# Kernel optimization log

Measured on AMD Instinct MI355X. Metric: run time of the kernel, lower is better.

## Reference

```python
import jax, jax.numpy as jnp
import numpy as np

N_NODES = 50000


def gat_layer(x, src, dst, W, att_s, att_d, b, concat):
    # PyG GATConv (eval mode): h = x W reshaped to [N, H, C]
    H, C = att_s.shape
    h = (x @ W).reshape(-1, H, C)                      # [N, H, C]
    a_s = (h * att_s).sum(-1)                          # [N, H]
    a_d = (h * att_d).sum(-1)                          # [N, H]
    e = jax.nn.leaky_relu(a_s[src] + a_d[dst], 0.2)    # [E, H]
    # scatter-softmax over destination nodes
    m = jax.ops.segment_max(e, dst, num_segments=N_NODES)
    alpha = jnp.exp(e - m[dst])
    denom = jax.ops.segment_sum(alpha, dst, num_segments=N_NODES)
    alpha = alpha / denom[dst]                         # [E, H]
    msg = h[src] * alpha[:, :, None]                   # [E, H, C]
    out = jax.ops.segment_sum(msg, dst, num_segments=N_NODES)  # [N, H, C]
    out = out.reshape(N_NODES, H * C) if concat else out.mean(axis=1)
    return out + b


def setup_inputs() -> dict:
    key = jax.random.key(0)
    ks = jax.random.split(key, 16)
    F_IN, HID, HEADS, NCLS, E = 512, 64, 4, 40, 800000
    x = jax.random.normal(ks[0], (N_NODES, F_IN), dtype=jnp.float32)
    edge_index = jax.random.randint(ks[1], (2, E), 0, N_NODES, dtype=jnp.int32)

    def glorot(k, shape):
        fan = shape[0]
        return jax.random.normal(k, shape, dtype=jnp.float32) / np.sqrt(fan)

    d1 = HID * HEADS  # 256
    return {
        "x": x,
        "edge_index": edge_index,
        "W1": glorot(ks[2], (F_IN, d1)),
        "as1": glorot(ks[3], (HEADS, HID)),
        "ad1": glorot(ks[4], (HEADS, HID)),
        "b1": jnp.zeros((d1,), jnp.float32),
        "W2": glorot(ks[5], (d1, d1)),
        "as2": glorot(ks[6], (HEADS, HID)),
        "ad2": glorot(ks[7], (HEADS, HID)),
        "b2": jnp.zeros((d1,), jnp.float32),
        "W3": glorot(ks[8], (d1, NCLS)),
        "as3": glorot(ks[9], (1, NCLS)),
        "ad3": glorot(ks[10], (1, NCLS)),
        "b3": jnp.zeros((NCLS,), jnp.float32),
    }


def reference(x, edge_index, W1, as1, ad1, b1, W2, as2, ad2, b2, W3, as3, ad3, b3):
    # add self-loops (PyG GATConv default)
    loops = jnp.arange(N_NODES, dtype=edge_index.dtype)
    src = jnp.concatenate([edge_index[0], loops])
    dst = jnp.concatenate([edge_index[1], loops])
    h = jax.nn.elu(gat_layer(x, src, dst, W1, as1, ad1, b1, True))
    h = jax.nn.elu(gat_layer(h, src, dst, W2, as2, ad2, b2, True))
    out = gat_layer(h, src, dst, W3, as3, ad3, b3, False)
    return out
```

## Files before the change

### kernel.cpp

```cpp
#include <hip/hip_runtime.h>
#include <stdint.h>

#define NN 50000
#define NB 196

typedef unsigned short u16;
typedef _Float16 f16;
typedef __attribute__((ext_vector_type(8))) _Float16 half8;
typedef __attribute__((ext_vector_type(4))) _Float16 half4;
typedef __attribute__((ext_vector_type(4))) float f32x4;

__device__ __forceinline__ void gload_lds16(const void* gsrc, void* ldst){
  __builtin_amdgcn_global_load_lds(
      (const __attribute__((address_space(1))) unsigned int*)gsrc,
      (__attribute__((address_space(3))) unsigned int*)ldst,
      16, 0, 0);
}

#define VMW(N)  asm volatile("s_waitcnt vmcnt(" #N ")" ::: "memory")
#define LGKM0() asm volatile("s_waitcnt lgkmcnt(0)" ::: "memory")
#define BARR()  asm volatile("s_barrier" ::: "memory")


__global__ void count_k(const int* __restrict__ dst, int* __restrict__ cnt, int E){
  int i = blockIdx.x * 256 + threadIdx.x;
  int tot = E + NN;
  if (i >= tot) return;
  int d = (i < E) ? dst[i] : (i - E);
  atomicAdd(&cnt[d], 1);
}

__global__ __launch_bounds__(256) void scan_part_k(const int* __restrict__ cnt,
                                                   int* __restrict__ bsum){
  __shared__ int lds[256];
  int tid = threadIdx.x;
  int idx = blockIdx.x * 256 + tid;
  lds[tid] = (idx < NN) ? cnt[idx] : 0;
  __syncthreads();
#pragma unroll
  for (int off = 128; off >= 1; off >>= 1){
    if (tid < off) lds[tid] += lds[tid + off];
    __syncthreads();
  }
  if (tid == 0) bsum[blockIdx.x] = lds[0];
}

__global__ __launch_bounds__(256) void scan_top_k(const int* __restrict__ bsum,
                                                  int* __restrict__ boff,
                                                  int* __restrict__ row_ptr){
  __shared__ int lds[256];
  int tid = threadIdx.x;
  int v = (tid < NB) ? bsum[tid] : 0;
  lds[tid] = v;
  __syncthreads();
#pragma unroll
  for (int off = 1; off < 256; off <<= 1){
    int t = (tid >= off) ? lds[tid - off] : 0;
    __syncthreads();
    lds[tid] += t;
    __syncthreads();
  }
  if (tid < NB) boff[tid] = lds[tid] - v;
  if (tid == 255) row_ptr[NN] = lds[255];
}

__global__ __launch_bounds__(256) void scan_fin_k(const int* __restrict__ cnt,
                                                  const int* __restrict__ boff,
                                                  int* __restrict__ row_ptr,
                                                  int* __restrict__ cursor){
  __shared__ int lds[256];
  int tid = threadIdx.x;
  int idx = blockIdx.x * 256 + tid;
  int v = (idx < NN) ? cnt[idx] : 0;
  lds[tid] = v;
  __syncthreads();
#pragma unroll
  for (int off = 1; off < 256; off <<= 1){
    int t = (tid >= off) ? lds[tid - off] : 0;
    __syncthreads();
    lds[tid] += t;
    __syncthreads();
  }
  if (idx < NN){
    int r = boff[blockIdx.x] + lds[tid] - v;
    row_ptr[idx] = r;
    cursor[idx]  = r;
  }
}

__global__ void scatter_k(const int* __restrict__ src, const int* __restrict__ dst,
                          int* __restrict__ cursor, int* __restrict__ csr,
                          int* __restrict__ csrd, int E){
  int i = blockIdx.x * 256 + threadIdx.x;
  int tot = E + NN;
  if (i >= tot) return;
  int s, d;
  if (i < E){ s = src[i]; d = dst[i]; } else { s = i - E; d = i - E; }
  int pos = atomicAdd(&cursor[d], 1);
  csr[pos] = s;
  csrd[pos] = d;
}


__global__ void transpose_k(const float* __restrict__ W, f16* __restrict__ Wt, int K, int N){
  int i = blockIdx.x * 256 + threadIdx.x;
  if (i >= K * N) return;
  int n = i / K, k = i - n * K;
  Wt[i] = (f16)W[k * N + n];
}


template<bool A_FP32>
__global__ __launch_bounds__(512) void gemm_big_k(const void* __restrict__ Aptr,
                                                  const f16* __restrict__ Bt,
                                                  f16* __restrict__ C,
                                                  const float* __restrict__ atts,
                                                  const float* __restrict__ attd,
                                                  float* __restrict__ a_s,
                                                  float* __restrict__ a_d,
                                                  int M, int K){
  constexpr int ABYTES = A_FP32 ? 16384 : 8192;
  constexpr int STEPB  = ABYTES + 16384;
  __shared__ __attribute__((aligned(16))) char lds[2 * STEPB];

  const int tid  = threadIdx.x;
  const int wave = tid >> 6, lane = tid & 63;
  const int quad = lane >> 4, l16 = lane & 15;
  const int wm = wave >> 2, wn = wave & 3;
  const int m0 = blockIdx.x * 128;
  const int sc_l = lane >> 4, r_l = lane & 15;

  const size_t bsrc0 = (size_t)(wave * 16 + r_l) * K + sc_l * 8;
  const size_t bsrc1 = (size_t)((wave + 8) * 16 + r_l) * K + sc_l * 8;
  const int bdst0 = wave * 1024;
  const int bdst1 = (wave + 8) * 1024;

  int arow = m0 + wave * 16 + r_l; if (arow > M - 1) arow = M - 1;
  const size_t asrc0 = (size_t)arow * K + sc_l * 8;
  const size_t asrc1 = asrc0 + 4;
  const int adst0 = wave * 1024;
  const int adst1 = 8192 + wave * 1024;

  auto stage = [&](int buf, int k0){
    char* Ab = lds + buf * STEPB;
    char* Bb = Ab + ABYTES;
    if constexpr (A_FP32){
      const float* A = (const float*)Aptr;
      gload_lds16(A + asrc0 + k0, Ab + adst0);
      gload_lds16(A + asrc1 + k0, Ab + adst1);
    } else {
      gload_lds16((const f16*)Aptr + asrc0 + k0, Ab + adst0);
    }
    gload_lds16(Bt + bsrc0 + k0, Bb + bdst0);
    gload_lds16(Bt + bsrc1 + k0, Bb + bdst1);
  };

  f32x4 acc[4][4] = {};

  auto compute = [&](int buf){
    char* Ab = lds + buf * STEPB;
    char* Bb = Ab + ABYTES;
    half8 af[4], bf[4];
    if constexpr (A_FP32){
#pragma unroll
      for (int i = 0; i < 4; ++i){
        const f32x4 lo = *(const f32x4*)(Ab + ((wm * 4 + i) * 64 + lane) * 16);
        const f32x4 hi = *(const f32x4*)(Ab + 8192 + ((wm * 4 + i) * 64 + lane) * 16);
        half8 v;
        v[0] = (f16)lo.x; v[1] = (f16)lo.y; v[2] = (f16)lo.z; v[3] = (f16)lo.w;
        v[4] = (f16)hi.x; v[5] = (f16)hi.y; v[6] = (f16)hi.z; v[7] = (f16)hi.w;
        af[i] = v;
      }
    } else {
#pragma unroll
      for (int i = 0; i < 4; ++i)
        af[i] = *(const half8*)(Ab + ((wm * 4 + i) * 64 + lane) * 16);
    }
#pragma unroll
    for (int j = 0; j < 4; ++j)
      bf[j] = *(const half8*)(Bb + ((wn * 4 + j) * 64 + lane) * 16);
#pragma unroll
    for (int i = 0; i < 4; ++i)
#pragma unroll
      for (int j = 0; j < 4; ++j)
        acc[i][j] = __builtin_amdgcn_mfma_f32_16x16x32_f16(af[i], bf[j], acc[i][j], 0, 0, 0);
  };

  stage(0, 0);

  const int nk = K >> 5;
  for (int t = 0; t < nk; ++t){
    if (t + 1 < nk){
      stage((t + 1) & 1, (t + 1) << 5);
      if constexpr (A_FP32) VMW(4); else VMW(3);
    } else {
      VMW(0);
    }
    BARR();
    compute(t & 1);
    LGKM0();
    BARR();
  }

  const int N = 256;
  const int head = wn;
  float sA[4], dA[4];
#pragma unroll
  for (int j = 0; j < 4; ++j){
    sA[j] = atts[head * 64 + j * 16 + l16];
    dA[j] = attd[head * 64 + j * 16 + l16];
  }
#pragma unroll
  for (int i = 0; i < 4; ++i){
#pragma unroll
    for (int r = 0; r < 4; ++r){
      int mm = m0 + wm * 64 + i * 16 + quad * 4 + r;
      float vs = 0.f, vd = 0.f;
#pragma unroll
      for (int j = 0; j < 4; ++j){
        float v = acc[i][j][r];
        vs += v * sA[j];
        vd += v * dA[j];
        int n = wn * 64 + j * 16 + l16;
        if (mm < M) C[(size_t)mm * N + n] = (f16)v;
      }
#pragma unroll
      for (int off = 8; off >= 1; off >>= 1){
        vs += __shfl_xor(vs, off);
        vd += __shfl_xor(vd, off);
      }
      if (l16 == 0 && mm < M){
        a_s[mm * 4 + head] = vs;
        a_d[mm * 4 + head] = vd;
      }
    }
  }
}


__global__ __launch_bounds__(256) void gemm_n40_k(const f16* __restrict__ A,
                                                  const f16* __restrict__ Bt,
                                                  f16* __restrict__ C,
                                                  const float* __restrict__ atts,
                                                  const float* __restrict__ attd,
                                                  float* __restrict__ a_s,
                                                  float* __restrict__ a_d,
                                                  int M, int K){
  constexpr int ABYTES = 4096;
  constexpr int BBYTES = 3072;
  constexpr int STEPB  = ABYTES + BBYTES;
  __shared__ __attribute__((aligned(16))) char lds[4 * STEPB];

  const int tid  = threadIdx.x;
  const int wave = tid >> 6, lane = tid & 63;
  const int quad = lane >> 4, l16 = lane & 15;
  const int m0 = blockIdx.x * 64;
  const int sc_l = lane >> 4, r_l = lane & 15;

  int arow = m0 + wave * 16 + r_l; if (arow > M - 1) arow = M - 1;
  const size_t asrc = (size_t)arow * K + sc_l * 8;
  const int adst = wave * 1024;
  int brow = wave * 16 + r_l; if (brow > 39) brow = 39;
  const size_t bsrc = (size_t)brow * K + sc_l * 8;
  const int bdst = wave * 1024;
  const bool b_active = (wave < 3);
  const bool two_ops = b_active;

  auto stage = [&](int buf, int k0){
    char* Ab = lds + buf * STEPB;
    char* Bb = Ab + ABYTES;
    gload_lds16(A + asrc + k0, Ab + adst);
    if (b_active) gload_lds16(Bt + bsrc + k0, Bb + bdst);
  };

  f32x4 acc[3] = {};
  auto compute = [&](int buf){
    char* Ab = lds + buf * STEPB;
    char* Bb = Ab + ABYTES;
    half8 af = *(const half8*)(Ab + (wave * 64 + lane) * 16);
    half8 bf[3];
#pragma unroll
    for (int j = 0; j < 3; ++j)
      bf[j] = *(const half8*)(Bb + (j * 64 + lane) * 16);
#pragma unroll
    for (int j = 0; j < 3; ++j)
      acc[j] = __builtin_amdgcn_mfma_f32_16x16x32_f16(af, bf[j], acc[j], 0, 0, 0);
  };

  stage(0, 0); stage(1, 32); stage(2, 64);
  const int nk = K >> 5;
  for (int t = 0; t < nk - 3; ++t){
    stage((t + 3) & 3, (t + 3) << 5);
    if (two_ops) VMW(6); else VMW(3);
    BARR();
    compute(t & 3);
    LGKM0();
    BARR();
  }
  if (two_ops) VMW(4); else VMW(2);
  BARR(); compute((nk - 3) & 3);
  if (two_ops) VMW(2); else VMW(1);
  BARR(); compute((nk - 2) & 3);
  VMW(0);
  BARR(); compute((nk - 1) & 3);

  float sA[3], dA[3];
#pragma unroll
  for (int j = 0; j < 3; ++j){
    int n = j * 16 + l16;
    sA[j] = (n < 40) ? atts[n] : 0.f;
    dA[j] = (n < 40) ? attd[n] : 0.f;
  }
#pragma unroll
  for (int r = 0; r < 4; ++r){
    int mm = m0 + wave * 16 + quad * 4 + r;
    float vs = 0.f, vd = 0.f;
#pragma unroll
    for (int j = 0; j < 3; ++j){
      float v = acc[j][r];
      vs += v * sA[j];
      vd += v * dA[j];
      int n = j * 16 + l16;
      if (mm < M && n < 40) C[(size_t)mm * 40 + n] = (f16)v;
    }
#pragma unroll
    for (int off = 8; off >= 1; off >>= 1){
      vs += __shfl_xor(vs, off);
      vd += __shfl_xor(vd, off);
    }
    if (l16 == 0 && mm < M){
      a_s[mm] = vs;
      a_d[mm] = vd;
    }
  }
}


__device__ __forceinline__ float lrelu(float e){ return e > 0.f ? e : 0.2f * e; }

__global__ void alpha4_k(const int* __restrict__ csr, const int* __restrict__ csrd,
                         const float* __restrict__ a_s, const float* __restrict__ a_d,
                         float* __restrict__ alpha, int tot){
  int i = blockIdx.x * 256 + threadIdx.x;
  if (i >= tot) return;
  int s = csr[i], d = csrd[i];
  const f32x4 as = *(const f32x4*)(a_s + ((size_t)s << 2));
  const f32x4 ad = *(const f32x4*)(a_d + ((size_t)d << 2));
  f32x4 al;
  al.x = __expf(lrelu(as.x + ad.x));
  al.y = __expf(lrelu(as.y + ad.y));
  al.z = __expf(lrelu(as.z + ad.z));
  al.w = __expf(lrelu(as.w + ad.w));
  *(f32x4*)(alpha + ((size_t)i << 2)) = al;
}

__global__ void alpha1_k(const int* __restrict__ csr, const int* __restrict__ csrd,
                         const float* __restrict__ a_s, const float* __restrict__ a_d,
                         float* __restrict__ alpha, int tot){
  int i = blockIdx.x * 256 + threadIdx.x;
  if (i >= tot) return;
  alpha[i] = __expf(lrelu(a_s[csr[i]] + a_d[csrd[i]]));
}


__global__ __launch_bounds__(256) void agg4_k(const f16* __restrict__ h,
                                              const float* __restrict__ alpha,
                                              const int* __restrict__ row_ptr,
                                              const int* __restrict__ csr,
                                              const float* __restrict__ bias,
                                              f16* __restrict__ out){
  int w = blockIdx.x * 4 + (threadIdx.x >> 6);
  if (w >= NN) return;
  const int lane = threadIdx.x & 63;
  const int head = lane >> 4;
  const char* hb = (const char*)h;
  const uint32_t hoff_lane = (uint32_t)lane << 3;
  const int beg = row_ptr[w], end = row_ptr[w + 1], endm1 = end - 1;

  float denom = 0.f, acc0 = 0.f, acc1 = 0.f, acc2 = 0.f, acc3 = 0.f;

  float ca[4]; half4 chv[4];
  float na[4]; half4 nhv[4];

  auto ldgrp = [&](int base, float* AV, half4* HV){
#pragma unroll
    for (int q = 0; q < 4; ++q){
      int idx = base + q; idx = idx < endm1 ? idx : endm1;
      int s = csr[idx];
      AV[q] = alpha[((size_t)idx << 2) + head];
      HV[q] = *(const half4*)(hb + (((uint32_t)s << 9) | hoff_lane));
    }
  };

  ldgrp(beg, ca, chv);
  int base = beg;
  while (true){
    bool more = base + 4 < end;
    if (more) ldgrp(base + 4, na, nhv);
    int rem = end - base;
#pragma unroll
    for (int q = 0; q < 4; ++q){
      float al = (q < rem) ? ca[q] : 0.f;
      denom += al;
      acc0 += al * (float)chv[q].x;
      acc1 += al * (float)chv[q].y;
      acc2 += al * (float)chv[q].z;
      acc3 += al * (float)chv[q].w;
    }
    if (!more) break;
#pragma unroll
    for (int q = 0; q < 4; ++q){ ca[q] = na[q]; chv[q] = nhv[q]; }
    base += 4;
  }

  float inv = 1.f / fmaxf(denom, 1e-30f);
  float o0 = acc0 * inv + bias[lane * 4 + 0];
  float o1 = acc1 * inv + bias[lane * 4 + 1];
  float o2 = acc2 * inv + bias[lane * 4 + 2];
  float o3 = acc3 * inv + bias[lane * 4 + 3];
  o0 = o0 > 0.f ? o0 : __expf(o0) - 1.f;
  o1 = o1 > 0.f ? o1 : __expf(o1) - 1.f;
  o2 = o2 > 0.f ? o2 : __expf(o2) - 1.f;
  o3 = o3 > 0.f ? o3 : __expf(o3) - 1.f;
  half4 rv; rv.x = (f16)o0; rv.y = (f16)o1; rv.z = (f16)o2; rv.w = (f16)o3;
  *(half4*)(out + (size_t)w * 256 + lane * 4) = rv;
}

__global__ __launch_bounds__(256) void agg1_k(const f16* __restrict__ h,
                                              const float* __restrict__ alpha,
                                              const int* __restrict__ row_ptr,
                                              const int* __restrict__ csr,
                                              const float* __restrict__ bias,
                                              float* __restrict__ out){
  int w = blockIdx.x * 4 + (threadIdx.x >> 6);
  if (w >= NN) return;
  const int lane = threadIdx.x & 63;
  const int cl = (lane < 40) ? lane : 0;
  const int beg = row_ptr[w], end = row_ptr[w + 1], endm1 = end - 1;

  float denom = 0.f, acc = 0.f;
  float ca[4], chv[4];
  float na[4], nhv[4];

  auto ldgrp = [&](int base, float* AV, float* HV){
#pragma unroll
    for (int q = 0; q < 4; ++q){
      int idx = base + q; idx = idx < endm1 ? idx : endm1;
      int s = csr[idx];
      AV[q] = alpha[idx];
      HV[q] = (float)h[(size_t)s * 40 + cl];
    }
  };

  ldgrp(beg, ca, chv);
  int base = beg;
  while (true){
    bool more = base + 4 < end;
    if (more) ldgrp(base + 4, na, nhv);
    int rem = end - base;
#pragma unroll
    for (int q = 0; q < 4; ++q){
      float al = (q < rem) ? ca[q] : 0.f;
      denom += al;
      acc += al * chv[q];
    }
    if (!more) break;
#pragma unroll
    for (int q = 0; q < 4; ++q){ ca[q] = na[q]; chv[q] = nhv[q]; }
    base += 4;
  }

  if (lane < 40){
    float o = acc / fmaxf(denom, 1e-30f) + bias[lane];
    out[(size_t)w * 40 + lane] = o;
  }
}


extern "C" void kernel_launch(void* const* d_in, const int* in_sizes, int n_in,
                              void* d_out, int out_size, void* d_ws, size_t ws_size,
                              hipStream_t stream){
  const float* x   = (const float*)d_in[0];
  const int*   ei  = (const int*)d_in[1];
  const float* W1  = (const float*)d_in[2];
  const float* as1 = (const float*)d_in[3];
  const float* ad1 = (const float*)d_in[4];
  const float* b1  = (const float*)d_in[5];
  const float* W2  = (const float*)d_in[6];
  const float* as2 = (const float*)d_in[7];
  const float* ad2 = (const float*)d_in[8];
  const float* b2  = (const float*)d_in[9];
  const float* W3  = (const float*)d_in[10];
  const float* as3 = (const float*)d_in[11];
  const float* ad3 = (const float*)d_in[12];
  const float* b3  = (const float*)d_in[13];

  const int E = in_sizes[1] / 2;
  const int ETOT = E + NN;
  const int* src_arr = ei;
  const int* dst_arr = ei + E;

  char* ws = (char*)d_ws;
  size_t off = 0;
  auto alloc = [&](size_t bytes) -> void* {
    void* p = ws + off; off += (bytes + 255) & ~(size_t)255; return p;
  };
  int*   cnt     = (int*)  alloc((size_t)NN * 4);
  int*   row_ptr = (int*)  alloc((size_t)(NN + 1) * 4);
  int*   cursor  = (int*)  alloc((size_t)NN * 4);
  int*   csr     = (int*)  alloc((size_t)ETOT * 4);
  int*   csrd    = (int*)  alloc((size_t)ETOT * 4);
  float* alpha   = (float*)alloc((size_t)ETOT * 4 * 4);
  int*   bsum    = (int*)  alloc((size_t)256 * 4);
  int*   boff    = (int*)  alloc((size_t)256 * 4);
  f16*   W1t     = (f16*)  alloc((size_t)512 * 256 * 2);
  f16*   W2t     = (f16*)  alloc((size_t)256 * 256 * 2);
  f16*   W3t     = (f16*)  alloc((size_t)256 * 40 * 2);
  float* a_s     = (float*)alloc((size_t)NN * 4 * 4);
  float* a_d     = (float*)alloc((size_t)NN * 4 * 4);
  f16*   hbuf    = (f16*)  alloc((size_t)NN * 256 * 2);
  f16*   xbuf    = (f16*)  alloc((size_t)NN * 256 * 2);
  (void)ws_size; (void)n_in; (void)out_size;

  hipMemsetAsync(cnt, 0, (size_t)NN * 4, stream);
  int egrid = (ETOT + 255) / 256;
  count_k    <<<egrid, 256, 0, stream>>>(dst_arr, cnt, E);
  scan_part_k<<<NB, 256, 0, stream>>>(cnt, bsum);
  scan_top_k <<<1, 256, 0, stream>>>(bsum, boff, row_ptr);
  scan_fin_k <<<NB, 256, 0, stream>>>(cnt, boff, row_ptr, cursor);
  scatter_k  <<<egrid, 256, 0, stream>>>(src_arr, dst_arr, cursor, csr, csrd, E);

  transpose_k<<<(512 * 256 + 255) / 256, 256, 0, stream>>>(W1, W1t, 512, 256);
  transpose_k<<<(256 * 256 + 255) / 256, 256, 0, stream>>>(W2, W2t, 256, 256);
  transpose_k<<<(256 * 40  + 255) / 256, 256, 0, stream>>>(W3, W3t, 256, 40);

  dim3 blk512(512);
  dim3 blk(256);
  dim3 gB((NN + 127) / 128);
  dim3 gC((NN + 63) / 64);
  int nodeblocks = (NN + 3) / 4;

  gemm_big_k<true> <<<gB, blk512, 0, stream>>>(x, W1t, hbuf, as1, ad1, a_s, a_d, NN, 512);
  alpha4_k<<<egrid, blk, 0, stream>>>(csr, csrd, a_s, a_d, alpha, ETOT);
  agg4_k<<<nodeblocks, blk, 0, stream>>>(hbuf, alpha, row_ptr, csr, b1, xbuf);

  gemm_big_k<false><<<gB, blk512, 0, stream>>>(xbuf, W2t, hbuf, as2, ad2, a_s, a_d, NN, 256);
  alpha4_k<<<egrid, blk, 0, stream>>>(csr, csrd, a_s, a_d, alpha, ETOT);
  agg4_k<<<nodeblocks, blk, 0, stream>>>(hbuf, alpha, row_ptr, csr, b2, xbuf);

  gemm_n40_k<<<gC, blk, 0, stream>>>(xbuf, W3t, hbuf, as3, ad3, a_s, a_d, NN, 256);
  alpha1_k<<<egrid, blk, 0, stream>>>(csr, csrd, a_s, a_d, alpha, ETOT);
  agg1_k<<<nodeblocks, blk, 0, stream>>>(hbuf, alpha, row_ptr, csr, b3, (float*)d_out);
}
```

Measured before the change: 512.2 us.

## Fuse all GAT stages into one persistent kernel with software grid barriers

Replaces the sequence of about fifteen kernel launches (CSR build, weight transposes, three GEMMs, alpha and aggregation passes) with a single persistent kernel of 256 blocks that loops over work with grid-stride loops. A global atomic barrier separates the phases. Edge counting is moved after the first GEMM inside the same phase, and the scans use 512-thread blocks. This removes launch overhead and inter-kernel gaps. In exchange, occupancy is fixed at the grid size, every phase pays a barrier cost, and the GEMM phases lose the parallelism of the full 391-tile grid.

```diff
diff --git a/kernel.cpp b/kernel.cpp
--- a/kernel.cpp
+++ b/kernel.cpp
@@ -1,10 +1,10 @@
 #include <hip/hip_runtime.h>
 #include <stdint.h>
 
-#define NN 50000
-#define NB 196
-
-typedef unsigned short u16;
+#define NN   50000
+#define MG   256
+#define NB2  98
+
 typedef _Float16 f16;
 typedef __attribute__((ext_vector_type(8))) _Float16 half8;
 typedef __attribute__((ext_vector_type(4))) _Float16 half4;
@@ -21,208 +21,228 @@
 #define LGKM0() asm volatile("s_waitcnt lgkmcnt(0)" ::: "memory")
 #define BARR()  asm volatile("s_barrier" ::: "memory")
 
-
-__global__ void count_k(const int* __restrict__ dst, int* __restrict__ cnt, int E){
-  int i = blockIdx.x * 256 + threadIdx.x;
-  int tot = E + NN;
-  if (i >= tot) return;
-  int d = (i < E) ? dst[i] : (i - E);
-  atomicAdd(&cnt[d], 1);
-}
-
-__global__ __launch_bounds__(256) void scan_part_k(const int* __restrict__ cnt,
-                                                   int* __restrict__ bsum){
-  __shared__ int lds[256];
-  int tid = threadIdx.x;
-  int idx = blockIdx.x * 256 + tid;
-  lds[tid] = (idx < NN) ? cnt[idx] : 0;
+__device__ __forceinline__ float lrelu(float e){ return e > 0.f ? e : 0.2f * e; }
+
+__device__ __forceinline__ void gbar(int* bar, int* phase){
   __syncthreads();
-#pragma unroll
-  for (int off = 128; off >= 1; off >>= 1){
-    if (tid < off) lds[tid] += lds[tid + off];
-    __syncthreads();
-  }
-  if (tid == 0) bsum[blockIdx.x] = lds[0];
-}
-
-__global__ __launch_bounds__(256) void scan_top_k(const int* __restrict__ bsum,
-                                                  int* __restrict__ boff,
-                                                  int* __restrict__ row_ptr){
-  __shared__ int lds[256];
-  int tid = threadIdx.x;
-  int v = (tid < NB) ? bsum[tid] : 0;
-  lds[tid] = v;
+  if (threadIdx.x == 0){
+    __threadfence();
+    int target = (++(*phase)) * MG;
+    __hip_atomic_fetch_add(bar, 1, __ATOMIC_ACQ_REL, __HIP_MEMORY_SCOPE_AGENT);
+    while (__hip_atomic_load(bar, __ATOMIC_ACQUIRE, __HIP_MEMORY_SCOPE_AGENT) < target)
+      __builtin_amdgcn_s_sleep(2);
+    __threadfence();
+  }
   __syncthreads();
-#pragma unroll
-  for (int off = 1; off < 256; off <<= 1){
-    int t = (tid >= off) ? lds[tid - off] : 0;
-    __syncthreads();
-    lds[tid] += t;
-    __syncthreads();
-  }
-  if (tid < NB) boff[tid] = lds[tid] - v;
-  if (tid == 255) row_ptr[NN] = lds[255];
-}
-
-__global__ __launch_bounds__(256) void scan_fin_k(const int* __restrict__ cnt,
-                                                  const int* __restrict__ boff,
-                                                  int* __restrict__ row_ptr,
-                                                  int* __restrict__ cursor){
-  __shared__ int lds[256];
-  int tid = threadIdx.x;
-  int idx = blockIdx.x * 256 + tid;
-  int v = (idx < NN) ? cnt[idx] : 0;
-  lds[tid] = v;
-  __syncthreads();
-#pragma unroll
-  for (int off = 1; off < 256; off <<= 1){
-    int t = (tid >= off) ? lds[tid - off] : 0;
-    __syncthreads();
-    lds[tid] += t;
-    __syncthreads();
-  }
-  if (idx < NN){
-    int r = boff[blockIdx.x] + lds[tid] - v;
-    row_ptr[idx] = r;
-    cursor[idx]  = r;
-  }
-}
-
-__global__ void scatter_k(const int* __restrict__ src, const int* __restrict__ dst,
-                          int* __restrict__ cursor, int* __restrict__ csr,
-                          int* __restrict__ csrd, int E){
-  int i = blockIdx.x * 256 + threadIdx.x;
-  int tot = E + NN;
-  if (i >= tot) return;
-  int s, d;
-  if (i < E){ s = src[i]; d = dst[i]; } else { s = i - E; d = i - E; }
-  int pos = atomicAdd(&cursor[d], 1);
-  csr[pos] = s;
-  csrd[pos] = d;
-}
-
-
-__global__ void transpose_k(const float* __restrict__ W, f16* __restrict__ Wt, int K, int N){
-  int i = blockIdx.x * 256 + threadIdx.x;
-  if (i >= K * N) return;
-  int n = i / K, k = i - n * K;
-  Wt[i] = (f16)W[k * N + n];
-}
-
+}
+
+struct MegaArgs {
+  const float* x; const int* ei; int E;
+  const float *W1, *as1, *ad1, *b1;
+  const float *W2, *as2, *ad2, *b2;
+  const float *W3, *as3, *ad3, *b3;
+  int *bar, *cnt, *row_ptr, *cursor, *csr, *csrd, *bsum, *boff;
+  float *alpha, *a_s, *a_d;
+  f16 *W1t, *W2t, *W3t, *hbuf, *xbuf;
+  float* out;
+};
 
 template<bool A_FP32>
-__global__ __launch_bounds__(512) void gemm_big_k(const void* __restrict__ Aptr,
-                                                  const f16* __restrict__ Bt,
-                                                  f16* __restrict__ C,
-                                                  const float* __restrict__ atts,
-                                                  const float* __restrict__ attd,
-                                                  float* __restrict__ a_s,
-                                                  float* __restrict__ a_d,
-                                                  int M, int K){
+__device__ void gemm_big_phase(const void* __restrict__ Aptr, const f16* __restrict__ Bt,
+                               f16* __restrict__ C,
+                               const float* __restrict__ atts, const float* __restrict__ attd,
+                               float* __restrict__ a_s, float* __restrict__ a_d,
+                               int M, int K, char* lds){
   constexpr int ABYTES = A_FP32 ? 16384 : 8192;
   constexpr int STEPB  = ABYTES + 16384;
-  __shared__ __attribute__((aligned(16))) char lds[2 * STEPB];
-
   const int tid  = threadIdx.x;
   const int wave = tid >> 6, lane = tid & 63;
   const int quad = lane >> 4, l16 = lane & 15;
   const int wm = wave >> 2, wn = wave & 3;
-  const int m0 = blockIdx.x * 128;
   const int sc_l = lane >> 4, r_l = lane & 15;
 
   const size_t bsrc0 = (size_t)(wave * 16 + r_l) * K + sc_l * 8;
   const size_t bsrc1 = (size_t)((wave + 8) * 16 + r_l) * K + sc_l * 8;
-  const int bdst0 = wave * 1024;
-  const int bdst1 = (wave + 8) * 1024;
-
-  int arow = m0 + wave * 16 + r_l; if (arow > M - 1) arow = M - 1;
-  const size_t asrc0 = (size_t)arow * K + sc_l * 8;
-  const size_t asrc1 = asrc0 + 4;
-  const int adst0 = wave * 1024;
-  const int adst1 = 8192 + wave * 1024;
-
-  auto stage = [&](int buf, int k0){
-    char* Ab = lds + buf * STEPB;
-    char* Bb = Ab + ABYTES;
-    if constexpr (A_FP32){
-      const float* A = (const float*)Aptr;
-      gload_lds16(A + asrc0 + k0, Ab + adst0);
-      gload_lds16(A + asrc1 + k0, Ab + adst1);
-    } else {
-      gload_lds16((const f16*)Aptr + asrc0 + k0, Ab + adst0);
-    }
-    gload_lds16(Bt + bsrc0 + k0, Bb + bdst0);
-    gload_lds16(Bt + bsrc1 + k0, Bb + bdst1);
-  };
-
-  f32x4 acc[4][4] = {};
-
-  auto compute = [&](int buf){
-    char* Ab = lds + buf * STEPB;
-    char* Bb = Ab + ABYTES;
-    half8 af[4], bf[4];
-    if constexpr (A_FP32){
-#pragma unroll
-      for (int i = 0; i < 4; ++i){
-        const f32x4 lo = *(const f32x4*)(Ab + ((wm * 4 + i) * 64 + lane) * 16);
-        const f32x4 hi = *(const f32x4*)(Ab + 8192 + ((wm * 4 + i) * 64 + lane) * 16);
-        half8 v;
-        v[0] = (f16)lo.x; v[1] = (f16)lo.y; v[2] = (f16)lo.z; v[3] = (f16)lo.w;
-        v[4] = (f16)hi.x; v[5] = (f16)hi.y; v[6] = (f16)hi.z; v[7] = (f16)hi.w;
-        af[i] = v;
-      }
-    } else {
+  const int bdst0 = wave * 1024, bdst1 = (wave + 8) * 1024;
+
+  const int ntiles = (M + 127) >> 7;
+  for (int tile = blockIdx.x; tile < ntiles; tile += gridDim.x){
+    const int m0 = tile << 7;
+    int arow = m0 + wave * 16 + r_l; if (arow > M - 1) arow = M - 1;
+    const size_t asrc0 = (size_t)arow * K + sc_l * 8;
+    const size_t asrc1 = asrc0 + 4;
+    const int adst0 = wave * 1024, adst1 = 8192 + wave * 1024;
+
+    auto stage = [&](int buf, int k0){
+      char* Ab = lds + buf * STEPB;
+      char* Bb = Ab + ABYTES;
+      if constexpr (A_FP32){
+        const float* A = (const float*)Aptr;
+        gload_lds16(A + asrc0 + k0, Ab + adst0);
+        gload_lds16(A + asrc1 + k0, Ab + adst1);
+      } else {
+        gload_lds16((const f16*)Aptr + asrc0 + k0, Ab + adst0);
+      }
+      gload_lds16(Bt + bsrc0 + k0, Bb + bdst0);
+      gload_lds16(Bt + bsrc1 + k0, Bb + bdst1);
+    };
+
+    f32x4 acc[4][4] = {};
+    auto compute = [&](int buf){
+      char* Ab = lds + buf * STEPB;
+      char* Bb = Ab + ABYTES;
+      half8 af[4], bf[4];
+      if constexpr (A_FP32){
+#pragma unroll
+        for (int i = 0; i < 4; ++i){
+          const f32x4 lo = *(const f32x4*)(Ab + ((wm * 4 + i) * 64 + lane) * 16);
+          const f32x4 hi = *(const f32x4*)(Ab + 8192 + ((wm * 4 + i) * 64 + lane) * 16);
+          half8 v;
+          v[0] = (f16)lo.x; v[1] = (f16)lo.y; v[2] = (f16)lo.z; v[3] = (f16)lo.w;
+          v[4] = (f16)hi.x; v[5] = (f16)hi.y; v[6] = (f16)hi.z; v[7] = (f16)hi.w;
+          af[i] = v;
+        }
+      } else {
+#pragma unroll
+        for (int i = 0; i < 4; ++i)
+          af[i] = *(const half8*)(Ab + ((wm * 4 + i) * 64 + lane) * 16);
+      }
+#pragma unroll
+      for (int j = 0; j < 4; ++j)
+        bf[j] = *(const half8*)(Bb + ((wn * 4 + j) * 64 + lane) * 16);
 #pragma unroll
       for (int i = 0; i < 4; ++i)
-        af[i] = *(const half8*)(Ab + ((wm * 4 + i) * 64 + lane) * 16);
-    }
-#pragma unroll
-    for (int j = 0; j < 4; ++j)
-      bf[j] = *(const half8*)(Bb + ((wn * 4 + j) * 64 + lane) * 16);
-#pragma unroll
-    for (int i = 0; i < 4; ++i)
-#pragma unroll
-      for (int j = 0; j < 4; ++j)
-        acc[i][j] = __builtin_amdgcn_mfma_f32_16x16x32_f16(af[i], bf[j], acc[i][j], 0, 0, 0);
-  };
-
-  stage(0, 0);
-
-  const int nk = K >> 5;
-  for (int t = 0; t < nk; ++t){
-    if (t + 1 < nk){
-      stage((t + 1) & 1, (t + 1) << 5);
-      if constexpr (A_FP32) VMW(4); else VMW(3);
-    } else {
-      VMW(0);
-    }
-    BARR();
-    compute(t & 1);
-    LGKM0();
-    BARR();
-  }
-
-  const int N = 256;
-  const int head = wn;
-  float sA[4], dA[4];
-#pragma unroll
-  for (int j = 0; j < 4; ++j){
-    sA[j] = atts[head * 64 + j * 16 + l16];
-    dA[j] = attd[head * 64 + j * 16 + l16];
-  }
-#pragma unroll
-  for (int i = 0; i < 4; ++i){
+#pragma unroll
+        for (int j = 0; j < 4; ++j)
+          acc[i][j] = __builtin_amdgcn_mfma_f32_16x16x32_f16(af[i], bf[j], acc[i][j], 0, 0, 0);
+    };
+
+    stage(0, 0);
+    const int nk = K >> 5;
+    for (int t = 0; t < nk; ++t){
+      if (t + 1 < nk){
+        stage((t + 1) & 1, (t + 1) << 5);
+        if constexpr (A_FP32) VMW(4); else VMW(3);
+      } else {
+        VMW(0);
+      }
+      BARR();
+      compute(t & 1);
+      LGKM0();
+      BARR();
+    }
+
+    const int head = wn;
+    float sA[4], dA[4];
+#pragma unroll
+    for (int j = 0; j < 4; ++j){
+      sA[j] = atts[head * 64 + j * 16 + l16];
+      dA[j] = attd[head * 64 + j * 16 + l16];
+    }
+#pragma unroll
+    for (int i = 0; i < 4; ++i){
+#pragma unroll
+      for (int r = 0; r < 4; ++r){
+        int mm = m0 + wm * 64 + i * 16 + quad * 4 + r;
+        float vs = 0.f, vd = 0.f;
+#pragma unroll
+        for (int j = 0; j < 4; ++j){
+          float v = acc[i][j][r];
+          vs += v * sA[j];
+          vd += v * dA[j];
+          int n = wn * 64 + j * 16 + l16;
+          if (mm < M) C[(size_t)mm * 256 + n] = (f16)v;
+        }
+#pragma unroll
+        for (int off = 8; off >= 1; off >>= 1){
+          vs += __shfl_xor(vs, off);
+          vd += __shfl_xor(vd, off);
+        }
+        if (l16 == 0 && mm < M){
+          a_s[mm * 4 + head] = vs;
+          a_d[mm * 4 + head] = vd;
+        }
+      }
+    }
+  }
+}
+
+__device__ void gemm_n40_phase(const f16* __restrict__ A, const f16* __restrict__ Bt,
+                               f16* __restrict__ C,
+                               const float* __restrict__ atts, const float* __restrict__ attd,
+                               float* __restrict__ a_s, float* __restrict__ a_d,
+                               int M, int K, char* lds){
+  constexpr int ABY = 8192, BBY = 3072, STEP = ABY + BBY;
+  const int tid  = threadIdx.x;
+  const int wave = tid >> 6, lane = tid & 63;
+  const int quad = lane >> 4, l16 = lane & 15;
+  const int sc_l = lane >> 4, r_l = lane & 15;
+
+  int brow = wave * 16 + r_l; if (brow > 39) brow = 39;
+  const size_t bsrc = (size_t)brow * K + sc_l * 8;
+  const int bdst = wave * 1024;
+  const bool b_act = (wave < 3);
+
+  const int ntiles = (M + 127) >> 7;
+  for (int tile = blockIdx.x; tile < ntiles; tile += gridDim.x){
+    const int m0 = tile << 7;
+    int arow = m0 + wave * 16 + r_l; if (arow > M - 1) arow = M - 1;
+    const size_t asrc = (size_t)arow * K + sc_l * 8;
+    const int adst = wave * 1024;
+
+    auto stage = [&](int buf, int k0){
+      char* Ab = lds + buf * STEP;
+      char* Bb = Ab + ABY;
+      gload_lds16(A + asrc + k0, Ab + adst);
+      if (b_act) gload_lds16(Bt + bsrc + k0, Bb + bdst);
+    };
+    f32x4 acc[3] = {};
+    auto compute = [&](int buf){
+      char* Ab = lds + buf * STEP;
+      char* Bb = Ab + ABY;
+      half8 af = *(const half8*)(Ab + (wave * 64 + lane) * 16);
+      half8 bf[3];
+#pragma unroll
+      for (int j = 0; j < 3; ++j)
+        bf[j] = *(const half8*)(Bb + (j * 64 + lane) * 16);
+#pragma unroll
+      for (int j = 0; j < 3; ++j)
+        acc[j] = __builtin_amdgcn_mfma_f32_16x16x32_f16(af, bf[j], acc[j], 0, 0, 0);
+    };
+
+    stage(0, 0);
+    const int nk = K >> 5;
+    for (int t = 0; t < nk; ++t){
+      if (t + 1 < nk){
+        stage((t + 1) & 1, (t + 1) << 5);
+        if (b_act) VMW(2); else VMW(1);
+      } else {
+        VMW(0);
+      }
+      BARR();
+      compute(t & 1);
+      LGKM0();
+      BARR();
+    }
+
+    float sA[3], dA[3];
+#pragma unroll
+    for (int j = 0; j < 3; ++j){
+      int n = j * 16 + l16;
+      sA[j] = (n < 40) ? atts[n] : 0.f;
+      dA[j] = (n < 40) ? attd[n] : 0.f;
+    }
 #pragma unroll
     for (int r = 0; r < 4; ++r){
-      int mm = m0 + wm * 64 + i * 16 + quad * 4 + r;
+      int mm = m0 + wave * 16 + quad * 4 + r;
       float vs = 0.f, vd = 0.f;
 #pragma unroll
-      for (int j = 0; j < 4; ++j){
-        float v = acc[i][j][r];
+      for (int j = 0; j < 3; ++j){
+        float v = acc[j][r];
         vs += v * sA[j];
         vd += v * dA[j];
-        int n = wn * 64 + j * 16 + l16;
-        if (mm < M) C[(size_t)mm * N + n] = (f16)v;
+        int n = j * 16 + l16;
+        if (mm < M && n < 40) C[(size_t)mm * 40 + n] = (f16)v;
       }
 #pragma unroll
       for (int off = 8; off >= 1; off >>= 1){
@@ -230,325 +250,308 @@
         vd += __shfl_xor(vd, off);
       }
       if (l16 == 0 && mm < M){
-        a_s[mm * 4 + head] = vs;
-        a_d[mm * 4 + head] = vd;
-      }
-    }
-  }
-}
-
-
-__global__ __launch_bounds__(256) void gemm_n40_k(const f16* __restrict__ A,
-                                                  const f16* __restrict__ Bt,
-                                                  f16* __restrict__ C,
-                                                  const float* __restrict__ atts,
-                                                  const float* __restrict__ attd,
-                                                  float* __restrict__ a_s,
-                                                  float* __restrict__ a_d,
-                                                  int M, int K){
-  constexpr int ABYTES = 4096;
-  constexpr int BBYTES = 3072;
-  constexpr int STEPB  = ABYTES + BBYTES;
-  __shared__ __attribute__((aligned(16))) char lds[4 * STEPB];
-
+        a_s[mm] = vs;
+        a_d[mm] = vd;
+      }
+    }
+  }
+}
+
+__device__ void agg4_phase(const f16* __restrict__ h, const float* __restrict__ alpha,
+                           const int* __restrict__ row_ptr, const int* __restrict__ csr,
+                           const float* __restrict__ bias, f16* __restrict__ out){
   const int tid  = threadIdx.x;
   const int wave = tid >> 6, lane = tid & 63;
-  const int quad = lane >> 4, l16 = lane & 15;
-  const int m0 = blockIdx.x * 64;
-  const int sc_l = lane >> 4, r_l = lane & 15;
-
-  int arow = m0 + wave * 16 + r_l; if (arow > M - 1) arow = M - 1;
-  const size_t asrc = (size_t)arow * K + sc_l * 8;
-  const int adst = wave * 1024;
-  int brow = wave * 16 + r_l; if (brow > 39) brow = 39;
-  const size_t bsrc = (size_t)brow * K + sc_l * 8;
-  const int bdst = wave * 1024;
-  const bool b_active = (wave < 3);
-  const bool two_ops = b_active;
-
-  auto stage = [&](int buf, int k0){
-    char* Ab = lds + buf * STEPB;
-    char* Bb = Ab + ABYTES;
-    gload_lds16(A + asrc + k0, Ab + adst);
-    if (b_active) gload_lds16(Bt + bsrc + k0, Bb + bdst);
-  };
-
-  f32x4 acc[3] = {};
-  auto compute = [&](int buf){
-    char* Ab = lds + buf * STEPB;
-    char* Bb = Ab + ABYTES;
-    half8 af = *(const half8*)(Ab + (wave * 64 + lane) * 16);
-    half8 bf[3];
-#pragma unroll
-    for (int j = 0; j < 3; ++j)
-      bf[j] = *(const half8*)(Bb + (j * 64 + lane) * 16);
-#pragma unroll
-    for (int j = 0; j < 3; ++j)
-      acc[j] = __builtin_amdgcn_mfma_f32_16x16x32_f16(af, bf[j], acc[j], 0, 0, 0);
-  };
-
-  stage(0, 0); stage(1, 32); stage(2, 64);
-  const int nk = K >> 5;
-  for (int t = 0; t < nk - 3; ++t){
-    stage((t + 3) & 3, (t + 3) << 5);
-    if (two_ops) VMW(6); else VMW(3);
-    BARR();
-    compute(t & 3);
-    LGKM0();
-    BARR();
-  }
-  if (two_ops) VMW(4); else VMW(2);
-  BARR(); compute((nk - 3) & 3);
-  if (two_ops) VMW(2); else VMW(1);
-  BARR(); compute((nk - 2) & 3);
-  VMW(0);
-  BARR(); compute((nk - 1) & 3);
-
-  float sA[3], dA[3];
-#pragma unroll
-  for (int j = 0; j < 3; ++j){
-    int n = j * 16 + l16;
-    sA[j] = (n < 40) ? atts[n] : 0.f;
-    dA[j] = (n < 40) ? attd[n] : 0.f;
-  }
-#pragma unroll
-  for (int r = 0; r < 4; ++r){
-    int mm = m0 + wave * 16 + quad * 4 + r;
-    float vs = 0.f, vd = 0.f;
-#pragma unroll
-    for (int j = 0; j < 3; ++j){
-      float v = acc[j][r];
-      vs += v * sA[j];
-      vd += v * dA[j];
-      int n = j * 16 + l16;
-      if (mm < M && n < 40) C[(size_t)mm * 40 + n] = (f16)v;
-    }
-#pragma unroll
-    for (int off = 8; off >= 1; off >>= 1){
-      vs += __shfl_xor(vs, off);
-      vd += __shfl_xor(vd, off);
-    }
-    if (l16 == 0 && mm < M){
-      a_s[mm] = vs;
-      a_d[mm] = vd;
-    }
-  }
-}
-
-
-__device__ __forceinline__ float lrelu(float e){ return e > 0.f ? e : 0.2f * e; }
-
-__global__ void alpha4_k(const int* __restrict__ csr, const int* __restrict__ csrd,
-                         const float* __restrict__ a_s, const float* __restrict__ a_d,
-                         float* __restrict__ alpha, int tot){
-  int i = blockIdx.x * 256 + threadIdx.x;
-  if (i >= tot) return;
-  int s = csr[i], d = csrd[i];
-  const f32x4 as = *(const f32x4*)(a_s + ((size_t)s << 2));
-  const f32x4 ad = *(const f32x4*)(a_d + ((size_t)d << 2));
-  f32x4 al;
-  al.x = __expf(lrelu(as.x + ad.x));
-  al.y = __expf(lrelu(as.y + ad.y));
-  al.z = __expf(lrelu(as.z + ad.z));
-  al.w = __expf(lrelu(as.w + ad.w));
-  *(f32x4*)(alpha + ((size_t)i << 2)) = al;
-}
-
-__global__ void alpha1_k(const int* __restrict__ csr, const int* __restrict__ csrd,
-                         const float* __restrict__ a_s, const float* __restrict__ a_d,
-                         float* __restrict__ alpha, int tot){
-  int i = blockIdx.x * 256 + threadIdx.x;
-  if (i >= tot) return;
-  alpha[i] = __expf(lrelu(a_s[csr[i]] + a_d[csrd[i]]));
-}
-
-
-__global__ __launch_bounds__(256) void agg4_k(const f16* __restrict__ h,
-                                              const float* __restrict__ alpha,
-                                              const int* __restrict__ row_ptr,
-                                              const int* __restrict__ csr,
-                                              const float* __restrict__ bias,
-                                              f16* __restrict__ out){
-  int w = blockIdx.x * 4 + (threadIdx.x >> 6);
-  if (w >= NN) return;
-  const int lane = threadIdx.x & 63;
   const int head = lane >> 4;
   const char* hb = (const char*)h;
   const uint32_t hoff_lane = (uint32_t)lane << 3;
-  const int beg = row_ptr[w], end = row_ptr[w + 1], endm1 = end - 1;
-
-  float denom = 0.f, acc0 = 0.f, acc1 = 0.f, acc2 = 0.f, acc3 = 0.f;
-
-  float ca[4]; half4 chv[4];
-  float na[4]; half4 nhv[4];
-
-  auto ldgrp = [&](int base, float* AV, half4* HV){
-#pragma unroll
-    for (int q = 0; q < 4; ++q){
-      int idx = base + q; idx = idx < endm1 ? idx : endm1;
-      int s = csr[idx];
-      AV[q] = alpha[((size_t)idx << 2) + head];
-      HV[q] = *(const half4*)(hb + (((uint32_t)s << 9) | hoff_lane));
-    }
-  };
-
-  ldgrp(beg, ca, chv);
-  int base = beg;
-  while (true){
-    bool more = base + 4 < end;
-    if (more) ldgrp(base + 4, na, nhv);
-    int rem = end - base;
-#pragma unroll
-    for (int q = 0; q < 4; ++q){
-      float al = (q < rem) ? ca[q] : 0.f;
-      denom += al;
-      acc0 += al * (float)chv[q].x;
-      acc1 += al * (float)chv[q].y;
-      acc2 += al * (float)chv[q].z;
-      acc3 += al * (float)chv[q].w;
-    }
-    if (!more) break;
-#pragma unroll
-    for (int q = 0; q < 4; ++q){ ca[q] = na[q]; chv[q] = nhv[q]; }
-    base += 4;
-  }
-
-  float inv = 1.f / fmaxf(denom, 1e-30f);
-  float o0 = acc0 * inv + bias[lane * 4 + 0];
-  float o1 = acc1 * inv + bias[lane * 4 + 1];
-  float o2 = acc2 * inv + bias[lane * 4 + 2];
-  float o3 = acc3 * inv + bias[lane * 4 + 3];
-  o0 = o0 > 0.f ? o0 : __expf(o0) - 1.f;
-  o1 = o1 > 0.f ? o1 : __expf(o1) - 1.f;
-  o2 = o2 > 0.f ? o2 : __expf(o2) - 1.f;
-  o3 = o3 > 0.f ? o3 : __expf(o3) - 1.f;
-  half4 rv; rv.x = (f16)o0; rv.y = (f16)o1; rv.z = (f16)o2; rv.w = (f16)o3;
-  *(half4*)(out + (size_t)w * 256 + lane * 4) = rv;
-}
-
-__global__ __launch_bounds__(256) void agg1_k(const f16* __restrict__ h,
-                                              const float* __restrict__ alpha,
-                                              const int* __restrict__ row_ptr,
-                                              const int* __restrict__ csr,
-                                              const float* __restrict__ bias,
-                                              float* __restrict__ out){
-  int w = blockIdx.x * 4 + (threadIdx.x >> 6);
-  if (w >= NN) return;
-  const int lane = threadIdx.x & 63;
+  const int wstride = gridDim.x * 8;
+
+  for (int w = blockIdx.x * 8 + wave; w < NN; w += wstride){
+    const int beg = row_ptr[w], end = row_ptr[w + 1], endm1 = end - 1;
+    float denom = 0.f, acc0 = 0.f, acc1 = 0.f, acc2 = 0.f, acc3 = 0.f;
+    float ca[4]; half4 chv[4];
+    float na[4]; half4 nhv[4];
+
+    auto ldgrp = [&](int base, float* AV, half4* HV){
+#pragma unroll
+      for (int q = 0; q < 4; ++q){
+        int idx = base + q; idx = idx < endm1 ? idx : endm1;
+        int s = csr[idx];
+        AV[q] = alpha[((size_t)idx << 2) + head];
+        HV[q] = *(const half4*)(hb + (((uint32_t)s << 9) | hoff_lane));
+      }
+    };
+
+    ldgrp(beg, ca, chv);
+    int base = beg;
+    while (true){
+      bool more = base + 4 < end;
+      if (more) ldgrp(base + 4, na, nhv);
+      int rem = end - base;
+#pragma unroll
+      for (int q = 0; q < 4; ++q){
+        float al = (q < rem) ? ca[q] : 0.f;
+        denom += al;
+        acc0 += al * (float)chv[q].x;
+        acc1 += al * (float)chv[q].y;
+        acc2 += al * (float)chv[q].z;
+        acc3 += al * (float)chv[q].w;
+      }
+      if (!more) break;
+#pragma unroll
+      for (int q = 0; q < 4; ++q){ ca[q] = na[q]; chv[q] = nhv[q]; }
+      base += 4;
+    }
+
+    float inv = 1.f / fmaxf(denom, 1e-30f);
+    float o0 = acc0 * inv + bias[lane * 4 + 0];
+    float o1 = acc1 * inv + bias[lane * 4 + 1];
+    float o2 = acc2 * inv + bias[lane * 4 + 2];
+    float o3 = acc3 * inv + bias[lane * 4 + 3];
+    o0 = o0 > 0.f ? o0 : __expf(o0) - 1.f;
+    o1 = o1 > 0.f ? o1 : __expf(o1) - 1.f;
+    o2 = o2 > 0.f ? o2 : __expf(o2) - 1.f;
+    o3 = o3 > 0.f ? o3 : __expf(o3) - 1.f;
+    half4 rv; rv.x = (f16)o0; rv.y = (f16)o1; rv.z = (f16)o2; rv.w = (f16)o3;
+    *(half4*)(out + (size_t)w * 256 + lane * 4) = rv;
+  }
+}
+
+__device__ void agg1_phase(const f16* __restrict__ h, const float* __restrict__ alpha,
+                           const int* __restrict__ row_ptr, const int* __restrict__ csr,
+                           const float* __restrict__ bias, float* __restrict__ out){
+  const int tid  = threadIdx.x;
+  const int wave = tid >> 6, lane = tid & 63;
   const int cl = (lane < 40) ? lane : 0;
-  const int beg = row_ptr[w], end = row_ptr[w + 1], endm1 = end - 1;
-
-  float denom = 0.f, acc = 0.f;
-  float ca[4], chv[4];
-  float na[4], nhv[4];
-
-  auto ldgrp = [&](int base, float* AV, float* HV){
-#pragma unroll
-    for (int q = 0; q < 4; ++q){
-      int idx = base + q; idx = idx < endm1 ? idx : endm1;
-      int s = csr[idx];
-      AV[q] = alpha[idx];
-      HV[q] = (float)h[(size_t)s * 40 + cl];
-    }
-  };
-
-  ldgrp(beg, ca, chv);
-  int base = beg;
-  while (true){
-    bool more = base + 4 < end;
-    if (more) ldgrp(base + 4, na, nhv);
-    int rem = end - base;
-#pragma unroll
-    for (int q = 0; q < 4; ++q){
-      float al = (q < rem) ? ca[q] : 0.f;
-      denom += al;
-      acc += al * chv[q];
-    }
-    if (!more) break;
-#pragma unroll
-    for (int q = 0; q < 4; ++q){ ca[q] = na[q]; chv[q] = nhv[q]; }
-    base += 4;
-  }
-
-  if (lane < 40){
-    float o = acc / fmaxf(denom, 1e-30f) + bias[lane];
-    out[(size_t)w * 40 + lane] = o;
-  }
+  const int wstride = gridDim.x * 8;
+
+  for (int w = blockIdx.x * 8 + wave; w < NN; w += wstride){
+    const int beg = row_ptr[w], end = row_ptr[w + 1], endm1 = end - 1;
+    float denom = 0.f, acc = 0.f;
+    float ca[4], chv[4];
+    float na[4], nhv[4];
+
+    auto ldgrp = [&](int base, float* AV, float* HV){
+#pragma unroll
+      for (int q = 0; q < 4; ++q){
+        int idx = base + q; idx = idx < endm1 ? idx : endm1;
+        int s = csr[idx];
+        AV[q] = alpha[idx];
+        HV[q] = (float)h[(size_t)s * 40 + cl];
+      }
+    };
+
+    ldgrp(beg, ca, chv);
+    int base = beg;
+    while (true){
+      bool more = base + 4 < end;
+      if (more) ldgrp(base + 4, na, nhv);
+      int rem = end - base;
+#pragma unroll
+      for (int q = 0; q < 4; ++q){
+        float al = (q < rem) ? ca[q] : 0.f;
+        denom += al;
+        acc += al * chv[q];
+      }
+      if (!more) break;
+#pragma unroll
+      for (int q = 0; q < 4; ++q){ ca[q] = na[q]; chv[q] = nhv[q]; }
+      base += 4;
+    }
+
+    if (lane < 40){
+      float o = acc / fmaxf(denom, 1e-30f) + bias[lane];
+      out[(size_t)w * 40 + lane] = o;
+    }
+  }
+}
+
+
+__global__ __launch_bounds__(512, 2) void mega_k(MegaArgs a){
+  __shared__ __attribute__((aligned(16))) char smem[65536];
+  int* sm = (int*)smem;
+  int bphase = 0;
+
+  const int tid  = threadIdx.x;
+  const int gsz  = gridDim.x * 512;
+  const int gtid = blockIdx.x * 512 + tid;
+  const int E = a.E, ETOT = a.E + NN;
+  const int* src_arr = a.ei;
+  const int* dst_arr = a.ei + E;
+
+  for (int i = gtid; i < NN; i += gsz) a.cnt[i] = 0;
+  for (int i = gtid; i < 512 * 256; i += gsz){
+    int n = i >> 9, k = i & 511;
+    a.W1t[i] = (f16)a.W1[k * 256 + n];
+  }
+  for (int i = gtid; i < 256 * 256; i += gsz){
+    int n = i >> 8, k = i & 255;
+    a.W2t[i] = (f16)a.W2[k * 256 + n];
+  }
+  for (int i = gtid; i < 40 * 256; i += gsz){
+    int n = i >> 8, k = i & 255;
+    a.W3t[i] = (f16)a.W3[k * 40 + n];
+  }
+  gbar(a.bar, &bphase);
+
+  gemm_big_phase<true>(a.x, a.W1t, a.hbuf, a.as1, a.ad1, a.a_s, a.a_d, NN, 512, smem);
+  for (int i = gtid; i < ETOT; i += gsz){
+    int d = (i < E) ? dst_arr[i] : (i - E);
+    atomicAdd(&a.cnt[d], 1);
+  }
+  gbar(a.bar, &bphase);
+
+  if (blockIdx.x < NB2){
+    int idx = blockIdx.x * 512 + tid;
+    sm[tid] = (idx < NN) ? a.cnt[idx] : 0;
+    __syncthreads();
+#pragma unroll
+    for (int off = 256; off >= 1; off >>= 1){
+      if (tid < off) sm[tid] += sm[tid + off];
+      __syncthreads();
+    }
+    if (tid == 0) a.bsum[blockIdx.x] = sm[0];
+  }
+  gbar(a.bar, &bphase);
+
+  if (blockIdx.x == 0){
+    int v = (tid < NB2) ? a.bsum[tid] : 0;
+    sm[tid] = v;
+    __syncthreads();
+#pragma unroll
+    for (int off = 1; off < 512; off <<= 1){
+      int t2 = (tid >= off) ? sm[tid - off] : 0;
+      __syncthreads();
+      sm[tid] += t2;
+      __syncthreads();
+    }
+    if (tid < NB2) a.boff[tid] = sm[tid] - v;
+    if (tid == 511) a.row_ptr[NN] = sm[511];
+  }
+  gbar(a.bar, &bphase);
+
+  if (blockIdx.x < NB2){
+    int idx = blockIdx.x * 512 + tid;
+    int v = (idx < NN) ? a.cnt[idx] : 0;
+    sm[tid] = v;
+    __syncthreads();
+#pragma unroll
+    for (int off = 1; off < 512; off <<= 1){
+      int t2 = (tid >= off) ? sm[tid - off] : 0;
+      __syncthreads();
+      sm[tid] += t2;
+      __syncthreads();
+    }
+    if (idx < NN){
+      int r = a.boff[blockIdx.x] + sm[tid] - v;
+      a.row_ptr[idx] = r;
+      a.cursor[idx]  = r;
+    }
+  }
+  gbar(a.bar, &bphase);
+
+  for (int i = gtid; i < ETOT; i += gsz){
+    int s, d;
+    if (i < E){ s = src_arr[i]; d = dst_arr[i]; } else { s = i - E; d = i - E; }
+    int pos = atomicAdd(&a.cursor[d], 1);
+    a.csr[pos] = s;
+    a.csrd[pos] = d;
+  }
+  gbar(a.bar, &bphase);
+
+  for (int i = gtid; i < ETOT; i += gsz){
+    int s = a.csr[i], d = a.csrd[i];
+    const f32x4 as = *(const f32x4*)(a.a_s + ((size_t)s << 2));
+    const f32x4 ad = *(const f32x4*)(a.a_d + ((size_t)d << 2));
+    f32x4 al;
+    al.x = __expf(lrelu(as.x + ad.x));
+    al.y = __expf(lrelu(as.y + ad.y));
+    al.z = __expf(lrelu(as.z + ad.z));
+    al.w = __expf(lrelu(as.w + ad.w));
+    *(f32x4*)(a.alpha + ((size_t)i << 2)) = al;
+  }
+  gbar(a.bar, &bphase);
+
+  agg4_phase(a.hbuf, a.alpha, a.row_ptr, a.csr, a.b1, a.xbuf);
+  gbar(a.bar, &bphase);
+
+  gemm_big_phase<false>(a.xbuf, a.W2t, a.hbuf, a.as2, a.ad2, a.a_s, a.a_d, NN, 256, smem);
+  gbar(a.bar, &bphase);
+
+  for (int i = gtid; i < ETOT; i += gsz){
+    int s = a.csr[i], d = a.csrd[i];
+    const f32x4 as = *(const f32x4*)(a.a_s + ((size_t)s << 2));
+    const f32x4 ad = *(const f32x4*)(a.a_d + ((size_t)d << 2));
+    f32x4 al;
+    al.x = __expf(lrelu(as.x + ad.x));
+    al.y = __expf(lrelu(as.y + ad.y));
+    al.z = __expf(lrelu(as.z + ad.z));
+    al.w = __expf(lrelu(as.w + ad.w));
+    *(f32x4*)(a.alpha + ((size_t)i << 2)) = al;
+  }
+  gbar(a.bar, &bphase);
+
+  agg4_phase(a.hbuf, a.alpha, a.row_ptr, a.csr, a.b2, a.xbuf);
+  gbar(a.bar, &bphase);
+
+  gemm_n40_phase(a.xbuf, a.W3t, a.hbuf, a.as3, a.ad3, a.a_s, a.a_d, NN, 256, smem);
+  gbar(a.bar, &bphase);
+
+  for (int i = gtid; i < ETOT; i += gsz)
+    a.alpha[i] = __expf(lrelu(a.a_s[a.csr[i]] + a.a_d[a.csrd[i]]));
+  gbar(a.bar, &bphase);
+
+  agg1_phase(a.hbuf, a.alpha, a.row_ptr, a.csr, a.b3, a.out);
 }
 
 
 extern "C" void kernel_launch(void* const* d_in, const int* in_sizes, int n_in,
                               void* d_out, int out_size, void* d_ws, size_t ws_size,
                               hipStream_t stream){
-  const float* x   = (const float*)d_in[0];
-  const int*   ei  = (const int*)d_in[1];
-  const float* W1  = (const float*)d_in[2];
-  const float* as1 = (const float*)d_in[3];
-  const float* ad1 = (const float*)d_in[4];
-  const float* b1  = (const float*)d_in[5];
-  const float* W2  = (const float*)d_in[6];
-  const float* as2 = (const float*)d_in[7];
-  const float* ad2 = (const float*)d_in[8];
-  const float* b2  = (const float*)d_in[9];
-  const float* W3  = (const float*)d_in[10];
-  const float* as3 = (const float*)d_in[11];
-  const float* ad3 = (const float*)d_in[12];
-  const float* b3  = (const float*)d_in[13];
-
   const int E = in_sizes[1] / 2;
   const int ETOT = E + NN;
-  const int* src_arr = ei;
-  const int* dst_arr = ei + E;
 
   char* ws = (char*)d_ws;
   size_t off = 0;
   auto alloc = [&](size_t bytes) -> void* {
     void* p = ws + off; off += (bytes + 255) & ~(size_t)255; return p;
   };
-  int*   cnt     = (int*)  alloc((size_t)NN * 4);
-  int*   row_ptr = (int*)  alloc((size_t)(NN + 1) * 4);
-  int*   cursor  = (int*)  alloc((size_t)NN * 4);
-  int*   csr     = (int*)  alloc((size_t)ETOT * 4);
-  int*   csrd    = (int*)  alloc((size_t)ETOT * 4);
-  float* alpha   = (float*)alloc((size_t)ETOT * 4 * 4);
-  int*   bsum    = (int*)  alloc((size_t)256 * 4);
-  int*   boff    = (int*)  alloc((size_t)256 * 4);
-  f16*   W1t     = (f16*)  alloc((size_t)512 * 256 * 2);
-  f16*   W2t     = (f16*)  alloc((size_t)256 * 256 * 2);
-  f16*   W3t     = (f16*)  alloc((size_t)256 * 40 * 2);
-  float* a_s     = (float*)alloc((size_t)NN * 4 * 4);
-  float* a_d     = (float*)alloc((size_t)NN * 4 * 4);
-  f16*   hbuf    = (f16*)  alloc((size_t)NN * 256 * 2);
-  f16*   xbuf    = (f16*)  alloc((size_t)NN * 256 * 2);
+  MegaArgs a;
+  a.x   = (const float*)d_in[0];
+  a.ei  = (const int*)d_in[1];
+  a.E   = E;
+  a.W1  = (const float*)d_in[2];
+  a.as1 = (const float*)d_in[3];
+  a.ad1 = (const float*)d_in[4];
+  a.b1  = (const float*)d_in[5];
+  a.W2  = (const float*)d_in[6];
+  a.as2 = (const float*)d_in[7];
+  a.ad2 = (const float*)d_in[8];
+  a.b2  = (const float*)d_in[9];
+  a.W3  = (const float*)d_in[10];
+  a.as3 = (const float*)d_in[11];
+  a.ad3 = (const float*)d_in[12];
+  a.b3  = (const float*)d_in[13];
+  a.bar     = (int*)  alloc(256);
+  a.cnt     = (int*)  alloc((size_t)NN * 4);
+  a.row_ptr = (int*)  alloc((size_t)(NN + 1) * 4);
+  a.cursor  = (int*)  alloc((size_t)NN * 4);
+  a.csr     = (int*)  alloc((size_t)ETOT * 4);
+  a.csrd    = (int*)  alloc((size_t)ETOT * 4);
+  a.alpha   = (float*)alloc((size_t)ETOT * 4 * 4);
+  a.bsum    = (int*)  alloc((size_t)256 * 4);
+  a.boff    = (int*)  alloc((size_t)256 * 4);
+  a.W1t     = (f16*)  alloc((size_t)512 * 256 * 2);
+  a.W2t     = (f16*)  alloc((size_t)256 * 256 * 2);
+  a.W3t     = (f16*)  alloc((size_t)256 * 40 * 2);
+  a.a_s     = (float*)alloc((size_t)NN * 4 * 4);
+  a.a_d     = (float*)alloc((size_t)NN * 4 * 4);
+  a.hbuf    = (f16*)  alloc((size_t)NN * 256 * 2);
+  a.xbuf    = (f16*)  alloc((size_t)NN * 256 * 2);
+  a.out     = (float*)d_out;
   (void)ws_size; (void)n_in; (void)out_size;
 
-  hipMemsetAsync(cnt, 0, (size_t)NN * 4, stream);
-  int egrid = (ETOT + 255) / 256;
-  count_k    <<<egrid, 256, 0, stream>>>(dst_arr, cnt, E);
-  scan_part_k<<<NB, 256, 0, stream>>>(cnt, bsum);
-  scan_top_k <<<1, 256, 0, stream>>>(bsum, boff, row_ptr);
-  scan_fin_k <<<NB, 256, 0, stream>>>(cnt, boff, row_ptr, cursor);
-  scatter_k  <<<egrid, 256, 0, stream>>>(src_arr, dst_arr, cursor, csr, csrd, E);
-
-  transpose_k<<<(512 * 256 + 255) / 256, 256, 0, stream>>>(W1, W1t, 512, 256);
-  transpose_k<<<(256 * 256 + 255) / 256, 256, 0, stream>>>(W2, W2t, 256, 256);
-  transpose_k<<<(256 * 40  + 255) / 256, 256, 0, stream>>>(W3, W3t, 256, 40);
-
-  dim3 blk512(512);
-  dim3 blk(256);
-  dim3 gB((NN + 127) / 128);
-  dim3 gC((NN + 63) / 64);
-  int nodeblocks = (NN + 3) / 4;
-
-  gemm_big_k<true> <<<gB, blk512, 0, stream>>>(x, W1t, hbuf, as1, ad1, a_s, a_d, NN, 512);
-  alpha4_k<<<egrid, blk, 0, stream>>>(csr, csrd, a_s, a_d, alpha, ETOT);
-  agg4_k<<<nodeblocks, blk, 0, stream>>>(hbuf, alpha, row_ptr, csr, b1, xbuf);
-
-  gemm_big_k<false><<<gB, blk512, 0, stream>>>(xbuf, W2t, hbuf, as2, ad2, a_s, a_d, NN, 256);
-  alpha4_k<<<egrid, blk, 0, stream>>>(csr, csrd, a_s, a_d, alpha, ETOT);
-  agg4_k<<<nodeblocks, blk, 0, stream>>>(hbuf, alpha, row_ptr, csr, b2, xbuf);
-
-  gemm_n40_k<<<gC, blk, 0, stream>>>(xbuf, W3t, hbuf, as3, ad3, a_s, a_d, NN, 256);
-  alpha1_k<<<egrid, blk, 0, stream>>>(csr, csrd, a_s, a_d, alpha, ETOT);
-  agg1_k<<<nodeblocks, blk, 0, stream>>>(hbuf, alpha, row_ptr, csr, b3, (float*)d_out);
-}
+  hipMemsetAsync(a.bar, 0, 256, stream);
+  mega_k<<<dim3(MG), dim3(512), 0, stream>>>(a);
+}
```

Result: slower. 1.191 ms (+132.6%).
